# Optimization experiments

Measured on AMD Instinct MI355X. Metric: run time of the kernel, lower is better.

Reference implementation:

```python
import jax, jax.numpy as jnp
import numpy as np

WINDOW = 9
REG_WEIGHT = 1.0


def _box_filter(x, k):
    """Sum over a k^3 box via three separable 1D ones-convs (== conv3d with ones kernel)."""
    pad = k // 2
    for ax in range(3):  # D, H, W spatial axes
        kshape = [1, 1, 1, 1, 1]
        kshape[2 + ax] = k
        kern = jnp.ones(kshape, x.dtype)
        padding = [(pad, pad) if i == ax else (0, 0) for i in range(3)]
        x = jax.lax.conv_general_dilated(
            x, kern, window_strides=(1, 1, 1), padding=padding,
            dimension_numbers=("NCDHW", "OIDHW", "NCDHW"))
    return x


def _ncc_loss(pred, target, k):
    win_size = jnp.asarray(float(k ** 3), pred.dtype)
    pred_sum = _box_filter(pred, k)
    target_sum = _box_filter(target, k)
    pred_sq_sum = _box_filter(pred * pred, k)
    target_sq_sum = _box_filter(target * target, k)
    pred_target_sum = _box_filter(pred * target, k)
    pred_mean = pred_sum / win_size
    target_mean = target_sum / win_size
    cross = (pred_target_sum - target_mean * pred_sum - pred_mean * target_sum
             + pred_mean * target_mean * win_size)
    pred_var = pred_sq_sum - 2.0 * pred_mean * pred_sum + pred_mean * pred_mean * win_size
    target_var = target_sq_sum - 2.0 * target_mean * target_sum + target_mean * target_mean * win_size
    pred_var = jnp.clip(pred_var, 0.0, None)
    target_var = jnp.clip(target_var, 0.0, None)
    cc = cross * cross / (pred_var * target_var + 0.001)
    cc = jnp.clip(cc, 0.0, 1.0)
    return 1.0 - jnp.mean(cc)


def _gradient_loss(flow):
    dy = jnp.abs(flow[:, :, 1:, :, :] - flow[:, :, :-1, :, :])
    dx = jnp.abs(flow[:, :, :, 1:, :] - flow[:, :, :, :-1, :])
    dz = jnp.abs(flow[:, :, :, :, 1:] - flow[:, :, :, :, :-1])
    return (jnp.mean(dy) + jnp.mean(dx) + jnp.mean(dz)) / 3.0


def setup_inputs() -> dict:
    key = jax.random.key(0)
    k1, k2, k3 = jax.random.split(key, 3)
    B, D, H, W = 2, 160, 160, 160
    moved = jax.random.uniform(k1, (B, 1, D, H, W), dtype=jnp.float32)
    fixed = jax.random.uniform(k2, (B, 1, D, H, W), dtype=jnp.float32)
    flow = jax.random.normal(k3, (B, 3, D, H, W), dtype=jnp.float32)
    return {"moved": moved, "fixed": fixed, "flow": flow}


def reference(moved, fixed, flow):
    sim_loss = _ncc_loss(moved, fixed, WINDOW)
    reg_loss = _gradient_loss(flow)
    total_loss = sim_loss + REG_WEIGHT * reg_loss
    return total_loss
```

## Files before the change

### kernel.cpp

```cpp
#include <hip/hip_runtime.h>

#define DD 160
#define HH 160
#define WW 160
#define VOL (DD * HH * WW)
#define PLANE (HH * WW)
#define NB 2

#define CH 32
#define NDSP (DD / CH)
#define DSBLK (PLANE / 256)
#define NDSUM (DSBLK * NDSP * NB)

#define GCHD 20
#define GBLK (NB * 3 * (DD / GCHD) * HH * (WW / 4) / 256)

#define HT 16
#define HS (HT + 8)
#define LDWH 168
#define WHBLK ((HH / HT) * DD * NB)

typedef _Float16 h8 __attribute__((ext_vector_type(8)));
typedef _Float16 h4 __attribute__((ext_vector_type(4)));

__global__ __launch_bounds__(256) void stream_pass(const float* __restrict__ mv,
                                                   const float* __restrict__ fx,
                                                   const float* __restrict__ fl,
                                                   _Float16* __restrict__ fields,
                                                   float* __restrict__ pg) {
    const int bx  = blockIdx.x;
    const int tid = threadIdx.x;

    if (bx < NDSUM) {
        const int hwb = bx % DSBLK;
        const int rem = bx / DSBLK;
        const int dsp = rem % NDSP;
        const int b   = rem / NDSP;
        const int hw  = hwb * 256 + tid;
        const int c0  = dsp * CH;

        const float* pm = mv + (size_t)b * VOL + hw;
        const float* pf = fx + (size_t)b * VOL + hw;
        _Float16*    fb = fields + (size_t)b * 5 * VOL + hw;

        float hm[9], hf[9];
        float s0 = 0.f, s1 = 0.f, s2 = 0.f, s3 = 0.f, s4 = 0.f;

#pragma unroll
        for (int jj = 0; jj < CH + 8; ++jj) {
            const int j = c0 - 4 + jj;
            if (jj >= 9) {
                float m = hm[jj % 9], f = hf[jj % 9];
                s0 -= m; s1 -= f;
                s2 -= m * m; s3 -= f * f; s4 -= m * f;
            }
            if (j >= 0 && j < DD) {
                float m = pm[(size_t)j * PLANE];
                float f = pf[(size_t)j * PLANE];
                s0 += m; s1 += f;
                s2 = fmaf(m, m, s2); s3 = fmaf(f, f, s3); s4 = fmaf(m, f, s4);
                hm[jj % 9] = m; hf[jj % 9] = f;
            } else {
                hm[jj % 9] = 0.f; hf[jj % 9] = 0.f;
            }
            if (jj >= 8) {
                const int dc = j - 4;
                _Float16* o = fb + (size_t)dc * PLANE;
                o[0 * (size_t)VOL] = (_Float16)s0;
                o[1 * (size_t)VOL] = (_Float16)s1;
                o[2 * (size_t)VOL] = (_Float16)s2;
                o[3 * (size_t)VOL] = (_Float16)s3;
                o[4 * (size_t)VOL] = (_Float16)s4;
            }
        }
        return;
    }

    const int gid = (bx - NDSUM) * 256 + tid;
    const int w4  = gid % 40;
    int t = gid / 40;
    const int h  = t % HH;  t /= HH;
    const int dc = t % (DD / GCHD); t /= (DD / GCHD);
    const int bc = t;
    const int d0 = dc * GCHD;
    const int w  = w4 * 4;

    const float* base = fl + (size_t)bc * VOL;
    float acc = 0.f;
    float4 v = *(const float4*)(base + ((size_t)d0 * HH + h) * WW + w);
    for (int d = d0; d < d0 + GCHD; ++d) {
        const float* pd = base + ((size_t)d * HH + h) * WW + w;
        float4 vn = v;
        if (d < DD - 1) {
            vn = *(const float4*)(pd + PLANE);
            acc += fabsf(vn.x - v.x) + fabsf(vn.y - v.y) +
                   fabsf(vn.z - v.z) + fabsf(vn.w - v.w);
        }
        if (h < HH - 1) {
            float4 vh = *(const float4*)(pd + WW);
            acc += fabsf(vh.x - v.x) + fabsf(vh.y - v.y) +
                   fabsf(vh.z - v.z) + fabsf(vh.w - v.w);
        }
        acc += fabsf(v.y - v.x) + fabsf(v.z - v.y) + fabsf(v.w - v.z);
        if (w < WW - 4) acc += fabsf(pd[4] - v.w);
        v = vn;
    }

    for (int o = 32; o > 0; o >>= 1) acc += __shfl_down(acc, o, 64);
    __shared__ float red[4];
    int lane = tid & 63, wid = tid >> 6;
    if (lane == 0) red[wid] = acc;
    __syncthreads();
    if (tid == 0) pg[bx - NDSUM] = red[0] + red[1] + red[2] + red[3];
}

__global__ __launch_bounds__(512, 6) void ncc_whcc(const _Float16* __restrict__ fields,
                                                   float* __restrict__ partial) {
    __shared__ _Float16 ws[5][HS][LDWH];
    __shared__ float red[8];

    const int hx  = blockIdx.x;
    const int d   = blockIdx.y;
    const int b   = blockIdx.z;
    const int h0  = hx * HT;
    const int tid = threadIdx.x;

    if (tid < 480) {
        const int r  = tid / 20;
        const int s  = tid - r * 20;
        const int h  = h0 - 4 + r;
        const int w0 = 8 * s;
        const bool rowok = (unsigned)h < (unsigned)HH;

#pragma unroll
        for (int f = 0; f < 5; ++f) {
            float v[16];
#pragma unroll
            for (int i = 0; i < 16; ++i) v[i] = 0.f;
            if (rowok) {
                const _Float16* fr = fields + (size_t)(b * 5 + f) * VOL
                                            + ((size_t)d * HH + h) * WW;
                if (s > 0) {
                    h4 a = *(const h4*)(fr + w0 - 4);
                    v[0] = (float)a.x; v[1] = (float)a.y; v[2] = (float)a.z; v[3] = (float)a.w;
                }
                h4 a1 = *(const h4*)(fr + w0);
                v[4] = (float)a1.x; v[5] = (float)a1.y; v[6] = (float)a1.z; v[7] = (float)a1.w;
                h4 a2 = *(const h4*)(fr + w0 + 4);
                v[8] = (float)a2.x; v[9] = (float)a2.y; v[10] = (float)a2.z; v[11] = (float)a2.w;
                if (s < 19) {
                    h4 a3 = *(const h4*)(fr + w0 + 8);
                    v[12] = (float)a3.x; v[13] = (float)a3.y; v[14] = (float)a3.z; v[15] = (float)a3.w;
                }
            }
            float o[8];
            float sum = 0.f;
#pragma unroll
            for (int i = 0; i < 9; ++i) sum += v[i];
            o[0] = sum;
#pragma unroll
            for (int k = 1; k < 8; ++k) {
                sum += v[k + 8] - v[k - 1];
                o[k] = sum;
            }
            h8 pk;
#pragma unroll
            for (int j = 0; j < 8; ++j) pk[j] = (_Float16)o[j];
            *(h8*)&ws[f][r][w0] = pk;
        }
    }
    __syncthreads();

    float acc = 0.f;
    if (tid < 320) {
        const int ro  = tid / 20;
        const int oct = tid - ro * 20;
        const int w   = 8 * oct;

        float s0[8], s1[8], s2[8], s3[8], s4[8];
#pragma unroll
        for (int j = 0; j < 8; ++j) { s0[j]=0.f; s1[j]=0.f; s2[j]=0.f; s3[j]=0.f; s4[j]=0.f; }
#pragma unroll
        for (int t = 0; t < 9; ++t) {
            h8 v0 = *(const h8*)&ws[0][ro + t][w];
            h8 v1 = *(const h8*)&ws[1][ro + t][w];
            h8 v2 = *(const h8*)&ws[2][ro + t][w];
            h8 v3 = *(const h8*)&ws[3][ro + t][w];
            h8 v4 = *(const h8*)&ws[4][ro + t][w];
#pragma unroll
            for (int j = 0; j < 8; ++j) {
                s0[j] += (float)v0[j]; s1[j] += (float)v1[j];
                s2[j] += (float)v2[j]; s3[j] += (float)v3[j];
                s4[j] += (float)v4[j];
            }
        }
        const float inv_win = 1.0f / 729.0f;
#pragma unroll
        for (int j = 0; j < 8; ++j) {
            float cross = fmaf(-(s0[j] * s1[j]), inv_win, s4[j]);
            float pv = fmaxf(fmaf(-(s0[j] * s0[j]), inv_win, s2[j]), 0.f);
            float tv = fmaxf(fmaf(-(s1[j] * s1[j]), inv_win, s3[j]), 0.f);
            float cc = cross * cross / (pv * tv + 0.001f);
            acc += fminf(fmaxf(cc, 0.f), 1.f);
        }
    }

    for (int o = 32; o > 0; o >>= 1) acc += __shfl_down(acc, o, 64);
    int lane = tid & 63, wid = tid >> 6;
    if (lane == 0) red[wid] = acc;
    __syncthreads();
    if (tid == 0) {
        float r8 = 0.f;
#pragma unroll
        for (int i = 0; i < 8; ++i) r8 += red[i];
        partial[((size_t)b * DD + d) * (HH / HT) + hx] = r8;
    }
}

__global__ __launch_bounds__(256) void finalize(const float* __restrict__ pcc, int ncc,
                                                const float* __restrict__ pg, int ng,
                                                float* __restrict__ out) {
    __shared__ float red[4];
    int lane = threadIdx.x & 63, wid = threadIdx.x >> 6;

    float a = 0.f;
    for (int i = threadIdx.x; i < ncc; i += 256) a += pcc[i];
    for (int o = 32; o > 0; o >>= 1) a += __shfl_down(a, o, 64);
    if (lane == 0) red[wid] = a;
    __syncthreads();
    float asum = red[0] + red[1] + red[2] + red[3];
    __syncthreads();

    float g = 0.f;
    for (int i = threadIdx.x; i < ng; i += 256) g += pg[i];
    for (int o = 32; o > 0; o >>= 1) g += __shfl_down(g, o, 64);
    if (lane == 0) red[wid] = g;
    __syncthreads();
    float gsum = red[0] + red[1] + red[2] + red[3];

    if (threadIdx.x == 0) {
        float sim = 1.0f - asum / 8192000.0f;
        float reg = gsum / 73267200.0f;
        out[0] = sim + reg;
    }
}

extern "C" void kernel_launch(void* const* d_in, const int* in_sizes, int n_in,
                              void* d_out, int out_size, void* d_ws, size_t ws_size,
                              hipStream_t stream) {
    const float* moved  = (const float*)d_in[0];
    const float* fixedp = (const float*)d_in[1];
    const float* flow   = (const float*)d_in[2];
    float* out = (float*)d_out;

    _Float16* fields = (_Float16*)d_ws;
    float* pcc = (float*)(fields + (size_t)NB * 5 * VOL);
    float* pg  = pcc + WHBLK;

    stream_pass<<<NDSUM + GBLK, 256, 0, stream>>>(moved, fixedp, flow, fields, pg);
    ncc_whcc<<<dim3(HH / HT, DD, NB), 512, 0, stream>>>(fields, pcc);
    finalize<<<1, 256, 0, stream>>>(pcc, WHBLK, pg, GBLK, out);
}
```

Baseline: 114.2 us.

## Vectorize D-axis box sum to float4 loads and half4 stores, shorten chunks

```diff
diff --git a/kernel.cpp b/kernel.cpp
--- a/kernel.cpp
+++ b/kernel.cpp
@@ -7,9 +7,9 @@
 #define PLANE (HH * WW)
 #define NB 2
 
-#define CH 32
+#define CH 20
 #define NDSP (DD / CH)
-#define DSBLK (PLANE / 256)
+#define DSBLK (PLANE / 1024)
 #define NDSUM (DSBLK * NDSP * NB)
 
 #define GCHD 20
@@ -32,47 +32,69 @@
     const int tid = threadIdx.x;
 
     if (bx < NDSUM) {
-        const int hwb = bx % DSBLK;
+        const int qt  = bx % DSBLK;
         const int rem = bx / DSBLK;
         const int dsp = rem % NDSP;
         const int b   = rem / NDSP;
-        const int hw  = hwb * 256 + tid;
+        const int hw  = (qt * 256 + tid) * 4;
         const int c0  = dsp * CH;
+        const int cend = c0 + CH;
 
         const float* pm = mv + (size_t)b * VOL + hw;
         const float* pf = fx + (size_t)b * VOL + hw;
         _Float16*    fb = fields + (size_t)b * 5 * VOL + hw;
 
-        float hm[9], hf[9];
-        float s0 = 0.f, s1 = 0.f, s2 = 0.f, s3 = 0.f, s4 = 0.f;
-
-#pragma unroll
-        for (int jj = 0; jj < CH + 8; ++jj) {
-            const int j = c0 - 4 + jj;
-            if (jj >= 9) {
-                float m = hm[jj % 9], f = hf[jj % 9];
-                s0 -= m; s1 -= f;
-                s2 -= m * m; s3 -= f * f; s4 -= m * f;
-            }
-            if (j >= 0 && j < DD) {
-                float m = pm[(size_t)j * PLANE];
-                float f = pf[(size_t)j * PLANE];
-                s0 += m; s1 += f;
-                s2 = fmaf(m, m, s2); s3 = fmaf(f, f, s3); s4 = fmaf(m, f, s4);
-                hm[jj % 9] = m; hf[jj % 9] = f;
-            } else {
-                hm[jj % 9] = 0.f; hf[jj % 9] = 0.f;
-            }
-            if (jj >= 8) {
-                const int dc = j - 4;
-                _Float16* o = fb + (size_t)dc * PLANE;
-                o[0 * (size_t)VOL] = (_Float16)s0;
-                o[1 * (size_t)VOL] = (_Float16)s1;
-                o[2 * (size_t)VOL] = (_Float16)s2;
-                o[3 * (size_t)VOL] = (_Float16)s3;
-                o[4 * (size_t)VOL] = (_Float16)s4;
-            }
-        }
+        float4 s0 = {0,0,0,0}, s1 = {0,0,0,0}, s2 = {0,0,0,0},
+               s3 = {0,0,0,0}, s4 = {0,0,0,0};
+
+#define ACC4(m4, f4, sgn)                                              \
+        s0.x sgn m4.x; s0.y sgn m4.y; s0.z sgn m4.z; s0.w sgn m4.w;    \
+        s1.x sgn f4.x; s1.y sgn f4.y; s1.z sgn f4.z; s1.w sgn f4.w;    \
+        s2.x sgn m4.x * m4.x; s2.y sgn m4.y * m4.y;                    \
+        s2.z sgn m4.z * m4.z; s2.w sgn m4.w * m4.w;                    \
+        s3.x sgn f4.x * f4.x; s3.y sgn f4.y * f4.y;                    \
+        s3.z sgn f4.z * f4.z; s3.w sgn f4.w * f4.w;                    \
+        s4.x sgn m4.x * f4.x; s4.y sgn m4.y * f4.y;                    \
+        s4.z sgn m4.z * f4.z; s4.w sgn m4.w * f4.w;
+
+        {
+            int lo = c0 - 4 > 0 ? c0 - 4 : 0;
+            int hi = c0 + 4 < DD - 1 ? c0 + 4 : DD - 1;
+            for (int dd = lo; dd <= hi; ++dd) {
+                float4 m4 = *(const float4*)(pm + (size_t)dd * PLANE);
+                float4 f4 = *(const float4*)(pf + (size_t)dd * PLANE);
+                ACC4(m4, f4, +=)
+            }
+        }
+
+        for (int d = c0; d < cend; ++d) {
+            _Float16* o = fb + (size_t)d * PLANE;
+            h4 t;
+            t.x = (_Float16)s0.x; t.y = (_Float16)s0.y; t.z = (_Float16)s0.z; t.w = (_Float16)s0.w;
+            *(h4*)(o + 0 * (size_t)VOL) = t;
+            t.x = (_Float16)s1.x; t.y = (_Float16)s1.y; t.z = (_Float16)s1.z; t.w = (_Float16)s1.w;
+            *(h4*)(o + 1 * (size_t)VOL) = t;
+            t.x = (_Float16)s2.x; t.y = (_Float16)s2.y; t.z = (_Float16)s2.z; t.w = (_Float16)s2.w;
+            *(h4*)(o + 2 * (size_t)VOL) = t;
+            t.x = (_Float16)s3.x; t.y = (_Float16)s3.y; t.z = (_Float16)s3.z; t.w = (_Float16)s3.w;
+            *(h4*)(o + 3 * (size_t)VOL) = t;
+            t.x = (_Float16)s4.x; t.y = (_Float16)s4.y; t.z = (_Float16)s4.z; t.w = (_Float16)s4.w;
+            *(h4*)(o + 4 * (size_t)VOL) = t;
+
+            if (d + 1 < cend) {
+                if (d + 5 < DD) {
+                    float4 m4 = *(const float4*)(pm + (size_t)(d + 5) * PLANE);
+                    float4 f4 = *(const float4*)(pf + (size_t)(d + 5) * PLANE);
+                    ACC4(m4, f4, +=)
+                }
+                if (d - 4 >= 0) {
+                    float4 m4 = *(const float4*)(pm + (size_t)(d - 4) * PLANE);
+                    float4 f4 = *(const float4*)(pf + (size_t)(d - 4) * PLANE);
+                    ACC4(m4, f4, -=)
+                }
+            }
+        }
+#undef ACC4
         return;
     }
 
```

Result: no change. 115.4 us (+1.1%).
